# Optimization experiments

Measured on AMD Instinct MI355X. Metric: run time of the kernel, lower is better.

## Reference

```python
import jax, jax.numpy as jnp
import numpy as np

B, C, H, W = 4, 64, 512, 512


def setup_inputs() -> dict:
    key = jax.random.key(0)
    k1, k2, k3 = jax.random.split(key, 3)
    z = jax.random.uniform(k1, (B, C, H, W), dtype=jnp.float32)      # gate in (0,1)
    h_tilde = jax.random.normal(k2, (B, C, H, W), dtype=jnp.float32)  # candidate state
    h0 = jax.random.normal(k3, (B, C, 1, W), dtype=jnp.float32)       # initial state row
    return {"z": z, "h_tilde": h_tilde, "h0": h0}


def reference(z, h_tilde, h0):
    # GruDirection2d with dh=1, dw=0 (forward_h): linear recurrence along H
    #   h[t] = z[t] * h_tilde[t] + (1 - z[t]) * h[t-1],  h[-1] = h0
    # Expressed as a single lax.scan over the H axis; each step is a fused
    # elementwise update on a [B, C, W] slice.
    zs = jnp.moveaxis(z, 2, 0)        # [H, B, C, W]
    hs = jnp.moveaxis(h_tilde, 2, 0)  # [H, B, C, W]

    def step(carry, inp):
        zt, ht = inp
        h = zt * ht + (1.0 - zt) * carry
        return h, h

    _, out = jax.lax.scan(step, h0[:, :, 0, :], (zs, hs))
    return jnp.moveaxis(out, 0, 2)    # [B, C, H, W]
```

## Files before the change

### kernel.cpp

```cpp
#include <hip/hip_runtime.h>


constexpr int Bc = 4;
constexpr int Cc = 64;
constexpr int Hc = 512;
constexpr int Wc = 512;

__global__ __launch_bounds__(256) void gru_h_scan(const float* __restrict__ z,
                                                  const float* __restrict__ ht,
                                                  const float* __restrict__ h0,
                                                  float* __restrict__ out) {
    const int cid = blockIdx.x * blockDim.x + threadIdx.x;
    const int bc = cid / Wc;
    const int w = cid - bc * Wc;

    const size_t base = (size_t)bc * Hc * Wc + w;

    float h = h0[(size_t)bc * Wc + w];

    const float* zp = z + base;
    const float* hp = ht + base;
    float* op = out + base;

#pragma unroll 16
    for (int t = 0; t < Hc; ++t) {
        const size_t off = (size_t)t * Wc;
        const float zt = zp[off];
        const float cd = hp[off];
        h = fmaf(zt, cd, (1.0f - zt) * h);
        __builtin_nontemporal_store(h, op + off);
    }
}

extern "C" void kernel_launch(void* const* d_in, const int* in_sizes, int n_in,
                              void* d_out, int out_size, void* d_ws, size_t ws_size,
                              hipStream_t stream) {
    const float* z = (const float*)d_in[0];
    const float* h_tilde = (const float*)d_in[1];
    const float* h0 = (const float*)d_in[2];
    float* out = (float*)d_out;

    const int n_chains = Bc * Cc * Wc;
    const int block = 256;
    const int grid = n_chains / block;
    gru_h_scan<<<grid, block, 0, stream>>>(z, h_tilde, h0, out);
}
```

Before: 152.1 us.

## Double-buffer row loads with inline-asm global loads and manual waitcnt

Replaces the simple unrolled time loop with a two-stage software pipeline. Blocks of 8 rows of z and h_tilde are fetched through inline-asm global_load_dword with immediate offsets, and explicit s_waitcnt / sched_barrier fences let the next block's loads overlap the current block's recurrence. The aim is to keep more memory requests in flight per thread and cut address arithmetic. In exchange it relies on hand-tuned vmcnt counts, which stores also increment on this architecture. It also drops the nontemporal store hint.

```diff
diff --git a/kernel.cpp b/kernel.cpp
--- a/kernel.cpp
+++ b/kernel.cpp
@@ -5,30 +5,84 @@
 constexpr int Cc = 64;
 constexpr int Hc = 512;
 constexpr int Wc = 512;
+constexpr int U  = 8;
+constexpr int NB = Hc / U;
+constexpr unsigned ROWB = Wc * sizeof(float);
+constexpr unsigned BLKB = U * ROWB;
+
+#define FENCE() __builtin_amdgcn_sched_barrier(0)
+
+#define GLOAD(dst, voff, sbase, imm) \
+    asm volatile("global_load_dword %0, %1, %2 offset:" #imm \
+                 : "=v"(dst) : "v"(voff), "s"(sbase))
 
 __global__ __launch_bounds__(256) void gru_h_scan(const float* __restrict__ z,
                                                   const float* __restrict__ ht,
                                                   const float* __restrict__ h0,
                                                   float* __restrict__ out) {
     const int cid = blockIdx.x * blockDim.x + threadIdx.x;
-    const int bc = cid / Wc;
-    const int w = cid - bc * Wc;
+    const int bc = cid >> 9;
+    const int w  = cid & (Wc - 1);
 
     const size_t base = (size_t)bc * Hc * Wc + w;
-
-    float h = h0[(size_t)bc * Wc + w];
-
-    const float* zp = z + base;
-    const float* hp = ht + base;
     float* op = out + base;
 
-#pragma unroll 16
-    for (int t = 0; t < Hc; ++t) {
-        const size_t off = (size_t)t * Wc;
-        const float zt = zp[off];
-        const float cd = hp[off];
-        h = fmaf(zt, cd, (1.0f - zt) * h);
-        __builtin_nontemporal_store(h, op + off);
+    float h;
+    {
+        unsigned hoff = (unsigned)((bc * Wc + w) * sizeof(float));
+        GLOAD(h, hoff, h0, 0);
+        asm volatile("s_waitcnt vmcnt(0)");
+        FENCE();
+    }
+
+    float zA[U], cA[U], zB[U], cB[U];
+    unsigned voff = (unsigned)(base * sizeof(float));
+
+    auto loadblk = [&](float (&zr)[U], float (&cr)[U], unsigned vo) {
+        const unsigned v1 = vo + 2 * ROWB, v2 = vo + 4 * ROWB, v3 = vo + 6 * ROWB;
+        GLOAD(zr[0], vo, z, 0);    GLOAD(zr[1], vo, z, 2048);
+        GLOAD(zr[2], v1, z, 0);    GLOAD(zr[3], v1, z, 2048);
+        GLOAD(zr[4], v2, z, 0);    GLOAD(zr[5], v2, z, 2048);
+        GLOAD(zr[6], v3, z, 0);    GLOAD(zr[7], v3, z, 2048);
+        GLOAD(cr[0], vo, ht, 0);   GLOAD(cr[1], vo, ht, 2048);
+        GLOAD(cr[2], v1, ht, 0);   GLOAD(cr[3], v1, ht, 2048);
+        GLOAD(cr[4], v2, ht, 0);   GLOAD(cr[5], v2, ht, 2048);
+        GLOAD(cr[6], v3, ht, 0);   GLOAD(cr[7], v3, ht, 2048);
+    };
+
+    auto computeblk = [&](float (&zr)[U], float (&cr)[U], int blk) {
+        const size_t roff = (size_t)blk * U * Wc;
+#pragma unroll
+        for (int i = 0; i < U; ++i) {
+            h = fmaf(zr[i], cr[i], (1.0f - zr[i]) * h);
+            op[roff + (size_t)i * Wc] = h;
+        }
+    };
+
+    loadblk(zA, cA, voff);
+    voff += BLKB;
+    FENCE();
+
+#pragma unroll 1
+    for (int b = 0; b < NB; b += 2) {
+        loadblk(zB, cB, voff);
+        voff += BLKB;
+        FENCE();
+        asm volatile("s_waitcnt vmcnt(16)");
+        FENCE();
+        computeblk(zA, cA, b);
+        FENCE();
+        if (b + 2 < NB) {
+            loadblk(zA, cA, voff);
+            voff += BLKB;
+            FENCE();
+            asm volatile("s_waitcnt vmcnt(16)");
+        } else {
+            asm volatile("s_waitcnt vmcnt(8)");
+        }
+        FENCE();
+        computeblk(zB, cB, b + 1);
+        FENCE();
     }
 }
 
```

Measured after the change: 156.4 us. 1.03x slower.

## Double-buffer z and h_tilde rows into LDS via async global_load_lds

Applied to the files above, without the earlier changes.

Each block now stages chunks of 8 rows of z and h_tilde into shared memory with direct global-to-LDS loads, double-buffered, so the next chunk's loads overlap the serial recurrence on the current chunk. Each wave loads 2 rows as 16-byte-per-lane vectors instead of each thread issuing scalar loads per step. The output store changes from a nontemporal store to a plain store. There is only one barrier per chunk, and nothing explicitly waits for the async LDS loads to finish before that barrier, so correctness depends on __syncthreads draining the vmcnt counter.

```diff
diff --git a/kernel.cpp b/kernel.cpp
--- a/kernel.cpp
+++ b/kernel.cpp
@@ -5,30 +5,57 @@
 constexpr int Cc = 64;
 constexpr int Hc = 512;
 constexpr int Wc = 512;
+constexpr int U  = 8;
+constexpr int NB = Hc / U;
 
 __global__ __launch_bounds__(256) void gru_h_scan(const float* __restrict__ z,
                                                   const float* __restrict__ ht,
                                                   const float* __restrict__ h0,
                                                   float* __restrict__ out) {
-    const int cid = blockIdx.x * blockDim.x + threadIdx.x;
-    const int bc = cid / Wc;
-    const int w = cid - bc * Wc;
+    __shared__ float smZ[2][U][256];
+    __shared__ float smH[2][U][256];
 
-    const size_t base = (size_t)bc * Hc * Wc + w;
+    const int tid  = threadIdx.x;
+    const int wid  = tid >> 6;
+    const int lane = tid & 63;
 
-    float h = h0[(size_t)bc * Wc + w];
+    const int bcblk = blockIdx.x >> 1;
+    const int wseg  = blockIdx.x & 1;
+    const size_t base = (size_t)bcblk * Hc * Wc + (size_t)wseg * 256;
 
-    const float* zp = z + base;
-    const float* hp = ht + base;
-    float* op = out + base;
+    const float* zb = z  + base;
+    const float* hb = ht + base;
+    float*       ob = out + base;
 
-#pragma unroll 16
-    for (int t = 0; t < Hc; ++t) {
-        const size_t off = (size_t)t * Wc;
-        const float zt = zp[off];
-        const float cd = hp[off];
-        h = fmaf(zt, cd, (1.0f - zt) * h);
-        __builtin_nontemporal_store(h, op + off);
+    float h = h0[(size_t)bcblk * Wc + wseg * 256 + tid];
+
+    auto stage = [&](int b, int buf) {
+        const int r0 = 2 * wid;
+#pragma unroll
+        for (int k = 0; k < 2; ++k) {
+            const int r = r0 + k;
+            const float* gz = zb + (size_t)(b * U + r) * Wc + lane * 4;
+            const float* gh = hb + (size_t)(b * U + r) * Wc + lane * 4;
+            __builtin_amdgcn_global_load_lds(gz, &smZ[buf][r][0], 16, 0, 0);
+            __builtin_amdgcn_global_load_lds(gh, &smH[buf][r][0], 16, 0, 0);
+        }
+    };
+
+    stage(0, 0);
+    __syncthreads();
+
+#pragma unroll 1
+    for (int b = 0; b < NB; ++b) {
+        const int buf = b & 1;
+        if (b + 1 < NB) stage(b + 1, buf ^ 1);
+#pragma unroll
+        for (int r = 0; r < U; ++r) {
+            const float zt = smZ[buf][r][tid];
+            const float cd = smH[buf][r][tid];
+            h = fmaf(zt, cd, (1.0f - zt) * h);
+            ob[(size_t)(b * U + r) * Wc + tid] = h;
+        }
+        __syncthreads();
     }
 }
 
@@ -40,8 +67,7 @@
     const float* h0 = (const float*)d_in[2];
     float* out = (float*)d_out;
 
-    const int n_chains = Bc * Cc * Wc;
+    const int grid = Bc * Cc * 2;
     const int block = 256;
-    const int grid = n_chains / block;
     gru_h_scan<<<grid, block, 0, stream>>>(z, h_tilde, h0, out);
 }
```

New measurement: 157.8 us. +3.8%, slower.
